# Kernel tuning notes

Measured on AMD Instinct MI355X. Metric: run time of the kernel, lower is better.

## Reference

```python
import jax, jax.numpy as jnp
import numpy as np

B, S, T, D = 16, 512, 16, 128
LN_EPS = 1e-5


def setup_inputs() -> dict:
    key = jax.random.key(0)
    k_x, k_h, k_w = jax.random.split(key, 3)
    x = jax.random.normal(k_x, (B, S, T, D), dtype=jnp.float32)
    # prev_hidden must be strictly positive (code takes its log)
    prev_hidden = jax.random.uniform(k_h, (B, 1, T, D), dtype=jnp.float32) * 0.9 + 0.05
    ln_gamma = jnp.ones((D,), jnp.float32)
    ln_beta = jnp.zeros((D,), jnp.float32)
    # torch Linear(dim, 2*dim): store as (D, 2D) for x @ W
    W = jax.random.normal(k_w, (D, 2 * D), dtype=jnp.float32) * (1.0 / np.sqrt(D))
    b = jnp.zeros((2 * D,), jnp.float32)
    return {"x": x, "prev_hidden": prev_hidden, "ln_gamma": ln_gamma,
            "ln_beta": ln_beta, "W": W, "b": b}


def _g_act_log(h):
    # log of G activation: x>=0 -> log(relu(x)+0.5); x<0 -> -softplus(-x)
    return jnp.where(h >= 0, jnp.log(jax.nn.relu(h) + 0.5), -jax.nn.softplus(-h))


def reference(x, prev_hidden, ln_gamma, ln_beta, W, b):
    seq_len = x.shape[1]
    # LayerNorm over last dim
    mu = jnp.mean(x, axis=-1, keepdims=True)
    var = jnp.var(x, axis=-1, keepdims=True)
    xn = (x - mu) * jax.lax.rsqrt(var + LN_EPS) * ln_gamma + ln_beta
    gh = jnp.einsum('bstd,de->bste', xn, W) + b  # (B,S,T,2D)
    gate, hidden = jnp.split(gh, 2, axis=-1)
    # parallel (seq_len > 1) log-space path
    log_coeffs = -jax.nn.softplus(gate)          # log(1 - z)
    log_z = -jax.nn.softplus(-gate)              # log z
    log_values = log_z + _g_act_log(hidden)      # (B,S,T,D)
    # prepend prev_hidden: values get log(h0), coeffs get zero pad
    log_values = jnp.concatenate([jnp.log(prev_hidden), log_values], axis=1)
    zero_pad = jnp.zeros_like(log_coeffs[:, :1])
    log_coeffs = jnp.concatenate([zero_pad, log_coeffs], axis=1)
    # Heinsen associative scan in log space
    a_star = jnp.cumsum(log_coeffs, axis=1)
    log_h0_plus_b_star = jax.lax.cumlogsumexp(log_values - a_star, axis=1)
    out = jnp.exp(a_star + log_h0_plus_b_star)
    out = out[:, -seq_len:]
    next_prev_hidden = out[:, -1:]
    return out, next_prev_hidden
```

## Files before the change

kernel.cpp:

```cpp
#include <hip/hip_runtime.h>
#include <hip/hip_bf16.h>
#include <stdint.h>

#define BB 16
#define SS 512
#define TT 16
#define DD 128
#define CH 64
#define NCH (SS/CH)
#define LN_EPS 1e-5f

typedef __attribute__((ext_vector_type(8))) short short8;
typedef __attribute__((ext_vector_type(4))) float f32x4;

static __device__ __forceinline__ uint32_t cvt_pk_bf16(float lo, float hi) {
    uint32_t r;
    asm("v_cvt_pk_bf16_f32 %0, %1, %2" : "=v"(r) : "v"(lo), "v"(hi));
    return r;
}

#define BAR() do {                                            \
    asm volatile("s_waitcnt lgkmcnt(0)" ::: "memory");        \
    __builtin_amdgcn_s_barrier();                             \
    asm volatile("" ::: "memory");                            \
} while (0)

__global__ __launch_bounds__(512, 2) void fused_mingru(
    const float* __restrict__ x, const float* __restrict__ prevh,
    const float* __restrict__ gamma, const float* __restrict__ beta,
    const float* __restrict__ W, const float* __restrict__ bias,
    float* __restrict__ out, float* __restrict__ nexth)
{
    __shared__ __align__(16) unsigned char xnb[2][CH*256];

    const int tid  = threadIdx.x;
    const int w    = tid >> 6;
    const int lane = tid & 63;
    const int l15  = lane & 15;
    const int lhi  = lane >> 4;

    const int bt = blockIdx.x;
    const size_t rowstride = (size_t)TT * DD;
    const size_t base_bt   = ((size_t)(bt >> 4) * SS * TT + (bt & 15)) * DD;

    const int r_ln = tid >> 3;
    const int c8   = tid & 7;
    const int slot_p = ((r_ln >> 2) & 3)*16 + (r_ln >> 4)*4 + (r_ln & 3);
    const int keyx   = slot_p & 7;
    const float* xp0 = x + base_bt + (size_t)r_ln * rowstride + c8*16;

    f32x4 px0, px1, px2, px3;
    auto issuePx = [&](int st) {
        const float* xp = xp0 + (size_t)st * CH * rowstride;
        px0 = *(const f32x4*)(xp + 0);
        px1 = *(const f32x4*)(xp + 4);
        px2 = *(const f32x4*)(xp + 8);
        px3 = *(const f32x4*)(xp + 12);
    };
    issuePx(0);

    short8 wfr[2][4];
    float  bs2[2];
    #pragma unroll
    for (int ni = 0; ni < 2; ++ni) {
        const int col = (ni ? 128 : 0) + w*16 + l15;
        float acc = 0.0f;
        #pragma unroll
        for (int kt = 0; kt < 4; ++kt) {
            union { short8 s8; uint32_t u[4]; } fr;
            #pragma unroll
            for (int p = 0; p < 4; ++p) {
                const int k0 = kt*32 + lhi*8 + 2*p;
                const float w0 = W[(size_t)k0*256 + col];
                const float w1 = W[(size_t)(k0+1)*256 + col];
                acc = fmaf(beta[k0],   w0, acc);
                acc = fmaf(beta[k0+1], w1, acc);
                fr.u[p] = cvt_pk_bf16(gamma[k0]*w0, gamma[k0+1]*w1);
            }
            wfr[ni][kt] = fr.s8;
        }
        acc += __shfl_xor(acc, 16);
        acc += __shfl_xor(acc, 32);
        bs2[ni] = bias[col] + acc;
    }

    float hM = prevh[(size_t)bt*128 + w*16 + l15];

    auto phaseLN = [&](int st) {
        float s1 = px0.x+px0.y+px0.z+px0.w + px1.x+px1.y+px1.z+px1.w
                 + px2.x+px2.y+px2.z+px2.w + px3.x+px3.y+px3.z+px3.w;
        float s2 = px0.x*px0.x+px0.y*px0.y+px0.z*px0.z+px0.w*px0.w
                 + px1.x*px1.x+px1.y*px1.y+px1.z*px1.z+px1.w*px1.w
                 + px2.x*px2.x+px2.y*px2.y+px2.z*px2.z+px2.w*px2.w
                 + px3.x*px3.x+px3.y*px3.y+px3.z*px3.z+px3.w*px3.w;
        s1 += __shfl_xor(s1, 1); s2 += __shfl_xor(s2, 1);
        s1 += __shfl_xor(s1, 2); s2 += __shfl_xor(s2, 2);
        s1 += __shfl_xor(s1, 4); s2 += __shfl_xor(s2, 4);
        const float mu = s1 * (1.0f/128.0f);
        const float rs = rsqrtf(s2 * (1.0f/128.0f) - mu*mu + LN_EPS);
        unsigned char* row = xnb[st & 1] + slot_p*256;
        union { short8 s8; uint32_t u[4]; } a, b2;
        a.u[0]  = cvt_pk_bf16((px0.x-mu)*rs, (px0.y-mu)*rs);
        a.u[1]  = cvt_pk_bf16((px0.z-mu)*rs, (px0.w-mu)*rs);
        a.u[2]  = cvt_pk_bf16((px1.x-mu)*rs, (px1.y-mu)*rs);
        a.u[3]  = cvt_pk_bf16((px1.z-mu)*rs, (px1.w-mu)*rs);
        b2.u[0] = cvt_pk_bf16((px2.x-mu)*rs, (px2.y-mu)*rs);
        b2.u[1] = cvt_pk_bf16((px2.z-mu)*rs, (px2.w-mu)*rs);
        b2.u[2] = cvt_pk_bf16((px3.x-mu)*rs, (px3.y-mu)*rs);
        b2.u[3] = cvt_pk_bf16((px3.z-mu)*rs, (px3.w-mu)*rs);
        *(short8*)(row + (((2*c8)     ^ keyx) << 4)) = a.s8;
        *(short8*)(row + (((2*c8 + 1) ^ keyx) << 4)) = b2.s8;
    };

    auto phaseG = [&](int st) {
        const unsigned char* xb = xnb[st & 1];
        float Cc[16], Cv[16];
        #pragma unroll
        for (int mt = 0; mt < 4; ++mt) {
            const unsigned char* rowp = xb + (mt*16 + l15)*256;
            short8 af[4];
            #pragma unroll
            for (int kt = 0; kt < 4; ++kt) {
                const int c = (kt << 2) | lhi;
                af[kt] = *(const short8*)(rowp + ((c ^ (l15 & 7)) << 4));
            }
            f32x4 ag = (f32x4)(0.f), ah = (f32x4)(0.f);
            #pragma unroll
            for (int kt = 0; kt < 4; ++kt) {
                ag = __builtin_amdgcn_mfma_f32_16x16x32_bf16(af[kt], wfr[0][kt], ag, 0, 0, 0);
                ah = __builtin_amdgcn_mfma_f32_16x16x32_bf16(af[kt], wfr[1][kt], ah, 0, 0, 0);
            }
            #pragma unroll
            for (int j = 0; j < 4; ++j) {
                const float g  = ag[j] + bs2[0];
                const float hh = ah[j] + bs2[1];
                const float cc = 1.0f / (1.0f + __expf(g));
                const float ga = (hh >= 0.0f) ? (hh + 0.5f)
                                              : (1.0f / (1.0f + __expf(-hh)));
                Cc[mt*4 + j] = cc;
                Cv[mt*4 + j] = (1.0f - cc) * ga;
            }
        }
        #pragma unroll
        for (int i = 1; i < 16; ++i) {
            Cv[i] = fmaf(Cc[i], Cv[i-1], Cv[i]);
            Cc[i] = Cc[i] * Cc[i-1];
        }
        float Ic = Cc[15], Iv = Cv[15];
        float pc = __shfl_up(Ic, 16), pv = __shfl_up(Iv, 16);
        if (lhi >= 1) { Iv = fmaf(Ic, pv, Iv); Ic *= pc; }
        pc = __shfl_up(Ic, 32); pv = __shfl_up(Iv, 32);
        if (lhi >= 2) { Iv = fmaf(Ic, pv, Iv); Ic *= pc; }
        float Ec = __shfl_up(Ic, 16), Ev = __shfl_up(Iv, 16);
        if (lhi == 0) { Ec = 1.0f; Ev = 0.0f; }
        const float Mc = __shfl(Ic, 48 + l15);
        const float Mv = __shfl(Iv, 48 + l15);
        const float hE = fmaf(Ec, hM, Ev);
        float* op = out + base_bt + (size_t)(st*CH + lhi*16) * rowstride + w*16 + l15;
        #pragma unroll
        for (int i = 0; i < 16; ++i)
            op[(size_t)i * rowstride] = fmaf(Cc[i], hE, Cv[i]);
        hM = fmaf(Mc, hM, Mv);
    };

    phaseLN(0);
    issuePx(1);
    BAR();

    for (int st = 0; st < NCH; ++st) {
        phaseG(st);
        if (st + 1 < NCH) {
            phaseLN(st + 1);
            if (st + 2 < NCH) issuePx(st + 2);
        }
        BAR();
    }

    if (lane < 16)
        nexth[(size_t)bt*128 + w*16 + lane] = hM;
}

extern "C" void kernel_launch(void* const* d_in, const int* in_sizes, int n_in,
                              void* d_out, int out_size, void* d_ws, size_t ws_size,
                              hipStream_t stream) {
    const float* x     = (const float*)d_in[0];
    const float* prevh = (const float*)d_in[1];
    const float* gamma = (const float*)d_in[2];
    const float* beta  = (const float*)d_in[3];
    const float* W     = (const float*)d_in[4];
    const float* bias  = (const float*)d_in[5];

    float* out   = (float*)d_out;
    float* nexth = out + (size_t)BB*SS*TT*DD;

    fused_mingru<<<BB*TT, 512, 0, stream>>>(x, prevh, gamma, beta, W, bias,
                                            out, nexth);
}
```

Before: 41.93 us.

## Software-pipeline chunk scan compute ahead of output tail with double-buffered packages

Splits the per-chunk work into a compute stage (MFMA, activations, intra-chunk scan) and a tail stage (apply carried hidden state and store outputs). Chunk s+1 is now computed before chunk s's tail runs, with results held in two alternating register packages. This breaks the serial dependence on hM so the stores and the next chunk's MFMA work can overlap. The change also switches to an explicit waves_per_eu(2,2) attribute and adds a sched_barrier after the x loads. It roughly doubles the live register state, which risks spills or lower occupancy.

```diff
diff --git a/kernel.cpp b/kernel.cpp
--- a/kernel.cpp
+++ b/kernel.cpp
@@ -25,7 +25,9 @@
     asm volatile("" ::: "memory");                            \
 } while (0)
 
-__global__ __launch_bounds__(512, 2) void fused_mingru(
+__global__ __launch_bounds__(512)
+__attribute__((amdgpu_waves_per_eu(2, 2)))
+void fused_mingru(
     const float* __restrict__ x, const float* __restrict__ prevh,
     const float* __restrict__ gamma, const float* __restrict__ beta,
     const float* __restrict__ W, const float* __restrict__ bias,
@@ -56,6 +58,7 @@
         px1 = *(const f32x4*)(xp + 4);
         px2 = *(const f32x4*)(xp + 8);
         px3 = *(const f32x4*)(xp + 12);
+        __builtin_amdgcn_sched_barrier(0);
     };
     issuePx(0);
 
@@ -112,9 +115,11 @@
         *(short8*)(row + (((2*c8 + 1) ^ keyx) << 4)) = b2.s8;
     };
 
-    auto phaseG = [&](int st) {
+    struct Pkg { float Cc[16], Cv[16], Ec, Ev, Mc, Mv; };
+    Pkg pkA, pkB;
+
+    auto computePkg = [&](int st, Pkg& P) {
         const unsigned char* xb = xnb[st & 1];
-        float Cc[16], Cv[16];
         #pragma unroll
         for (int mt = 0; mt < 4; ++mt) {
             const unsigned char* rowp = xb + (mt*16 + l15)*256;
@@ -137,42 +142,55 @@
                 const float cc = 1.0f / (1.0f + __expf(g));
                 const float ga = (hh >= 0.0f) ? (hh + 0.5f)
                                               : (1.0f / (1.0f + __expf(-hh)));
-                Cc[mt*4 + j] = cc;
-                Cv[mt*4 + j] = (1.0f - cc) * ga;
+                P.Cc[mt*4 + j] = cc;
+                P.Cv[mt*4 + j] = (1.0f - cc) * ga;
             }
         }
         #pragma unroll
         for (int i = 1; i < 16; ++i) {
-            Cv[i] = fmaf(Cc[i], Cv[i-1], Cv[i]);
-            Cc[i] = Cc[i] * Cc[i-1];
+            P.Cv[i] = fmaf(P.Cc[i], P.Cv[i-1], P.Cv[i]);
+            P.Cc[i] = P.Cc[i] * P.Cc[i-1];
         }
-        float Ic = Cc[15], Iv = Cv[15];
+        float Ic = P.Cc[15], Iv = P.Cv[15];
         float pc = __shfl_up(Ic, 16), pv = __shfl_up(Iv, 16);
         if (lhi >= 1) { Iv = fmaf(Ic, pv, Iv); Ic *= pc; }
         pc = __shfl_up(Ic, 32); pv = __shfl_up(Iv, 32);
         if (lhi >= 2) { Iv = fmaf(Ic, pv, Iv); Ic *= pc; }
         float Ec = __shfl_up(Ic, 16), Ev = __shfl_up(Iv, 16);
         if (lhi == 0) { Ec = 1.0f; Ev = 0.0f; }
-        const float Mc = __shfl(Ic, 48 + l15);
-        const float Mv = __shfl(Iv, 48 + l15);
-        const float hE = fmaf(Ec, hM, Ev);
+        P.Ec = Ec; P.Ev = Ev;
+        P.Mc = __shfl(Ic, 48 + l15);
+        P.Mv = __shfl(Iv, 48 + l15);
+    };
+
+    auto tail = [&](int st, Pkg& P) {
+        const float hE = fmaf(P.Ec, hM, P.Ev);
         float* op = out + base_bt + (size_t)(st*CH + lhi*16) * rowstride + w*16 + l15;
         #pragma unroll
         for (int i = 0; i < 16; ++i)
-            op[(size_t)i * rowstride] = fmaf(Cc[i], hE, Cv[i]);
-        hM = fmaf(Mc, hM, Mv);
+            op[(size_t)i * rowstride] = fmaf(P.Cc[i], hE, P.Cv[i]);
+        hM = fmaf(P.Mc, hM, P.Mv);
     };
 
     phaseLN(0);
     issuePx(1);
     BAR();
-
-    for (int st = 0; st < NCH; ++st) {
-        phaseG(st);
-        if (st + 1 < NCH) {
-            phaseLN(st + 1);
-            if (st + 2 < NCH) issuePx(st + 2);
-        }
+    computePkg(0, pkA);
+    phaseLN(1);
+    issuePx(2);
+    BAR();
+
+    #pragma unroll
+    for (int s2 = 0; s2 < NCH; s2 += 2) {
+        if (s2 + 1 < NCH) computePkg(s2 + 1, pkB);
+        tail(s2, pkA);
+        if (s2 + 2 < NCH) phaseLN(s2 + 2);
+        if (s2 + 3 < NCH) issuePx(s2 + 3);
+        BAR();
+        if (s2 + 2 < NCH) computePkg(s2 + 2, pkA);
+        tail(s2 + 1, pkB);
+        if (s2 + 3 < NCH) phaseLN(s2 + 3);
+        if (s2 + 4 < NCH) issuePx(s2 + 4);
         BAR();
     }
 
```

Measured after the change: 42.46 us. About the same (+1.3%).

## Split each (b,t) sequence across two 256-thread blocks by output-column half

Applied to the files above, without the earlier changes.

Each (b,t) scan is now handled by two blocks of 256 threads, each computing 64 of the 128 output channels, doubling the grid to 512 blocks. Every block still loads and LayerNorms the full 64-row x chunk, with 4 threads per row and 32 floats each, so x reads and LN work are duplicated. The aim is more blocks to fill the 256 CUs and less serial work per block, at the cost of twice the x traffic and more registers per thread for the larger LN load.

```diff
diff --git a/kernel.cpp b/kernel.cpp
--- a/kernel.cpp
+++ b/kernel.cpp
@@ -25,7 +25,7 @@
     asm volatile("" ::: "memory");                            \
 } while (0)
 
-__global__ __launch_bounds__(512, 2) void fused_mingru(
+__global__ __launch_bounds__(256, 2) void fused_mingru(
     const float* __restrict__ x, const float* __restrict__ prevh,
     const float* __restrict__ gamma, const float* __restrict__ beta,
     const float* __restrict__ W, const float* __restrict__ bias,
@@ -39,23 +39,23 @@
     const int l15  = lane & 15;
     const int lhi  = lane >> 4;
 
-    const int bt = blockIdx.x;
+    const int bt   = blockIdx.x >> 1;
+    const int half = blockIdx.x & 1;
     const size_t rowstride = (size_t)TT * DD;
     const size_t base_bt   = ((size_t)(bt >> 4) * SS * TT + (bt & 15)) * DD;
 
-    const int r_ln = tid >> 3;
-    const int c8   = tid & 7;
+    const int r_ln = tid >> 2;
+    const int c4   = tid & 3;
     const int slot_p = ((r_ln >> 2) & 3)*16 + (r_ln >> 4)*4 + (r_ln & 3);
     const int keyx   = slot_p & 7;
-    const float* xp0 = x + base_bt + (size_t)r_ln * rowstride + c8*16;
+    const float* xp0 = x + base_bt + (size_t)r_ln * rowstride + c4*32;
 
-    f32x4 px0, px1, px2, px3;
+    f32x4 px[8];
     auto issuePx = [&](int st) {
         const float* xp = xp0 + (size_t)st * CH * rowstride;
-        px0 = *(const f32x4*)(xp + 0);
-        px1 = *(const f32x4*)(xp + 4);
-        px2 = *(const f32x4*)(xp + 8);
-        px3 = *(const f32x4*)(xp + 12);
+        #pragma unroll
+        for (int q = 0; q < 8; ++q)
+            px[q] = *(const f32x4*)(xp + q*4);
     };
     issuePx(0);
 
@@ -63,7 +63,7 @@
     float  bs2[2];
     #pragma unroll
     for (int ni = 0; ni < 2; ++ni) {
-        const int col = (ni ? 128 : 0) + w*16 + l15;
+        const int col = (ni ? 128 : 0) + half*64 + w*16 + l15;
         float acc = 0.0f;
         #pragma unroll
         for (int kt = 0; kt < 4; ++kt) {
@@ -84,32 +84,31 @@
         bs2[ni] = bias[col] + acc;
     }
 
-    float hM = prevh[(size_t)bt*128 + w*16 + l15];
+    float hM = prevh[(size_t)bt*128 + half*64 + w*16 + l15];
 
     auto phaseLN = [&](int st) {
-        float s1 = px0.x+px0.y+px0.z+px0.w + px1.x+px1.y+px1.z+px1.w
-                 + px2.x+px2.y+px2.z+px2.w + px3.x+px3.y+px3.z+px3.w;
-        float s2 = px0.x*px0.x+px0.y*px0.y+px0.z*px0.z+px0.w*px0.w
-                 + px1.x*px1.x+px1.y*px1.y+px1.z*px1.z+px1.w*px1.w
-                 + px2.x*px2.x+px2.y*px2.y+px2.z*px2.z+px2.w*px2.w
-                 + px3.x*px3.x+px3.y*px3.y+px3.z*px3.z+px3.w*px3.w;
+        float s1 = 0.f, s2 = 0.f;
+        #pragma unroll
+        for (int q = 0; q < 8; ++q) {
+            s1 += px[q].x + px[q].y + px[q].z + px[q].w;
+            s2 += px[q].x*px[q].x + px[q].y*px[q].y
+                + px[q].z*px[q].z + px[q].w*px[q].w;
+        }
         s1 += __shfl_xor(s1, 1); s2 += __shfl_xor(s2, 1);
         s1 += __shfl_xor(s1, 2); s2 += __shfl_xor(s2, 2);
-        s1 += __shfl_xor(s1, 4); s2 += __shfl_xor(s2, 4);
         const float mu = s1 * (1.0f/128.0f);
         const float rs = rsqrtf(s2 * (1.0f/128.0f) - mu*mu + LN_EPS);
         unsigned char* row = xnb[st & 1] + slot_p*256;
-        union { short8 s8; uint32_t u[4]; } a, b2;
-        a.u[0]  = cvt_pk_bf16((px0.x-mu)*rs, (px0.y-mu)*rs);
-        a.u[1]  = cvt_pk_bf16((px0.z-mu)*rs, (px0.w-mu)*rs);
-        a.u[2]  = cvt_pk_bf16((px1.x-mu)*rs, (px1.y-mu)*rs);
-        a.u[3]  = cvt_pk_bf16((px1.z-mu)*rs, (px1.w-mu)*rs);
-        b2.u[0] = cvt_pk_bf16((px2.x-mu)*rs, (px2.y-mu)*rs);
-        b2.u[1] = cvt_pk_bf16((px2.z-mu)*rs, (px2.w-mu)*rs);
-        b2.u[2] = cvt_pk_bf16((px3.x-mu)*rs, (px3.y-mu)*rs);
-        b2.u[3] = cvt_pk_bf16((px3.z-mu)*rs, (px3.w-mu)*rs);
-        *(short8*)(row + (((2*c8)     ^ keyx) << 4)) = a.s8;
-        *(short8*)(row + (((2*c8 + 1) ^ keyx) << 4)) = b2.s8;
+        #pragma unroll
+        for (int m = 0; m < 4; ++m) {
+            union { short8 s8; uint32_t u[4]; } a;
+            a.u[0] = cvt_pk_bf16((px[2*m].x  -mu)*rs, (px[2*m].y  -mu)*rs);
+            a.u[1] = cvt_pk_bf16((px[2*m].z  -mu)*rs, (px[2*m].w  -mu)*rs);
+            a.u[2] = cvt_pk_bf16((px[2*m+1].x-mu)*rs, (px[2*m+1].y-mu)*rs);
+            a.u[3] = cvt_pk_bf16((px[2*m+1].z-mu)*rs, (px[2*m+1].w-mu)*rs);
+            const int ci = c4*4 + m;
+            *(short8*)(row + ((ci ^ keyx) << 4)) = a.s8;
+        }
     };
 
     auto phaseG = [&](int st) {
@@ -156,7 +155,8 @@
         const float Mc = __shfl(Ic, 48 + l15);
         const float Mv = __shfl(Iv, 48 + l15);
         const float hE = fmaf(Ec, hM, Ev);
-        float* op = out + base_bt + (size_t)(st*CH + lhi*16) * rowstride + w*16 + l15;
+        float* op = out + base_bt + (size_t)(st*CH + lhi*16) * rowstride
+                  + half*64 + w*16 + l15;
         #pragma unroll
         for (int i = 0; i < 16; ++i)
             op[(size_t)i * rowstride] = fmaf(Cc[i], hE, Cv[i]);
@@ -177,7 +177,7 @@
     }
 
     if (lane < 16)
-        nexth[(size_t)bt*128 + w*16 + lane] = hM;
+        nexth[(size_t)bt*128 + half*64 + w*16 + lane] = hM;
 }
 
 extern "C" void kernel_launch(void* const* d_in, const int* in_sizes, int n_in,
@@ -193,6 +193,6 @@
     float* out   = (float*)d_out;
     float* nexth = out + (size_t)BB*SS*TT*DD;
 
-    fused_mingru<<<BB*TT, 512, 0, stream>>>(x, prevh, gamma, beta, W, bias,
-                                            out, nexth);
+    fused_mingru<<<BB*TT*2, 256, 0, stream>>>(x, prevh, gamma, beta, W, bias,
+                                              out, nexth);
 }
```

New measurement: 51.54 us. +22.9%, slower.

## Split each chunk's scan across two wave groups with 1024-thread blocks

Applied to the files above, without the earlier changes.

Blocks grow from 512 to 1024 threads. The two groups of 8 waves each handle half of a 64-row chunk: 32 rows each, with 8 scan steps per lane instead of 16. The chunk carry is exchanged through a small shared buffer, and a second barrier per chunk resolves the cross-group prefix. This halves per-thread serial work and register pressure so more waves can hide latency with only 256 blocks in the grid, at the cost of an extra barrier per chunk and redundant W fragment loads per group.

```diff
diff --git a/kernel.cpp b/kernel.cpp
--- a/kernel.cpp
+++ b/kernel.cpp
@@ -25,16 +25,19 @@
     asm volatile("" ::: "memory");                            \
 } while (0)
 
-__global__ __launch_bounds__(512, 2) void fused_mingru(
+__global__ __launch_bounds__(1024, 4) void fused_mingru(
     const float* __restrict__ x, const float* __restrict__ prevh,
     const float* __restrict__ gamma, const float* __restrict__ beta,
     const float* __restrict__ W, const float* __restrict__ bias,
     float* __restrict__ out, float* __restrict__ nexth)
 {
     __shared__ __align__(16) unsigned char xnb[2][CH*256];
+    __shared__ float2 Mex[2][8][16];
 
     const int tid  = threadIdx.x;
-    const int w    = tid >> 6;
+    const int wave = tid >> 6;
+    const int q    = wave >> 3;
+    const int w    = wave & 7;
     const int lane = tid & 63;
     const int l15  = lane & 15;
     const int lhi  = lane >> 4;
@@ -43,19 +46,19 @@
     const size_t rowstride = (size_t)TT * DD;
     const size_t base_bt   = ((size_t)(bt >> 4) * SS * TT + (bt & 15)) * DD;
 
-    const int r_ln = tid >> 3;
-    const int c8   = tid & 7;
-    const int slot_p = ((r_ln >> 2) & 3)*16 + (r_ln >> 4)*4 + (r_ln & 3);
+    const int r_ln = tid >> 4;
+    const int c16  = tid & 15;
+    const int remq = r_ln & 31;
+    const int slot_p = ((r_ln >> 5)*2 + ((remq >> 2) & 1))*16
+                     + (remq >> 3)*4 + (remq & 3);
     const int keyx   = slot_p & 7;
-    const float* xp0 = x + base_bt + (size_t)r_ln * rowstride + c8*16;
-
-    f32x4 px0, px1, px2, px3;
+    const float* xp0 = x + base_bt + (size_t)r_ln * rowstride + c16*8;
+
+    f32x4 pxa, pxb;
     auto issuePx = [&](int st) {
         const float* xp = xp0 + (size_t)st * CH * rowstride;
-        px0 = *(const f32x4*)(xp + 0);
-        px1 = *(const f32x4*)(xp + 4);
-        px2 = *(const f32x4*)(xp + 8);
-        px3 = *(const f32x4*)(xp + 12);
+        pxa = *(const f32x4*)(xp + 0);
+        pxb = *(const f32x4*)(xp + 4);
     };
     issuePx(0);
 
@@ -87,37 +90,30 @@
     float hM = prevh[(size_t)bt*128 + w*16 + l15];
 
     auto phaseLN = [&](int st) {
-        float s1 = px0.x+px0.y+px0.z+px0.w + px1.x+px1.y+px1.z+px1.w
-                 + px2.x+px2.y+px2.z+px2.w + px3.x+px3.y+px3.z+px3.w;
-        float s2 = px0.x*px0.x+px0.y*px0.y+px0.z*px0.z+px0.w*px0.w
-                 + px1.x*px1.x+px1.y*px1.y+px1.z*px1.z+px1.w*px1.w
-                 + px2.x*px2.x+px2.y*px2.y+px2.z*px2.z+px2.w*px2.w
-                 + px3.x*px3.x+px3.y*px3.y+px3.z*px3.z+px3.w*px3.w;
+        float s1 = pxa.x+pxa.y+pxa.z+pxa.w + pxb.x+pxb.y+pxb.z+pxb.w;
+        float s2 = pxa.x*pxa.x+pxa.y*pxa.y+pxa.z*pxa.z+pxa.w*pxa.w
+                 + pxb.x*pxb.x+pxb.y*pxb.y+pxb.z*pxb.z+pxb.w*pxb.w;
         s1 += __shfl_xor(s1, 1); s2 += __shfl_xor(s2, 1);
         s1 += __shfl_xor(s1, 2); s2 += __shfl_xor(s2, 2);
         s1 += __shfl_xor(s1, 4); s2 += __shfl_xor(s2, 4);
+        s1 += __shfl_xor(s1, 8); s2 += __shfl_xor(s2, 8);
         const float mu = s1 * (1.0f/128.0f);
         const float rs = rsqrtf(s2 * (1.0f/128.0f) - mu*mu + LN_EPS);
-        unsigned char* row = xnb[st & 1] + slot_p*256;
-        union { short8 s8; uint32_t u[4]; } a, b2;
-        a.u[0]  = cvt_pk_bf16((px0.x-mu)*rs, (px0.y-mu)*rs);
-        a.u[1]  = cvt_pk_bf16((px0.z-mu)*rs, (px0.w-mu)*rs);
-        a.u[2]  = cvt_pk_bf16((px1.x-mu)*rs, (px1.y-mu)*rs);
-        a.u[3]  = cvt_pk_bf16((px1.z-mu)*rs, (px1.w-mu)*rs);
-        b2.u[0] = cvt_pk_bf16((px2.x-mu)*rs, (px2.y-mu)*rs);
-        b2.u[1] = cvt_pk_bf16((px2.z-mu)*rs, (px2.w-mu)*rs);
-        b2.u[2] = cvt_pk_bf16((px3.x-mu)*rs, (px3.y-mu)*rs);
-        b2.u[3] = cvt_pk_bf16((px3.z-mu)*rs, (px3.w-mu)*rs);
-        *(short8*)(row + (((2*c8)     ^ keyx) << 4)) = a.s8;
-        *(short8*)(row + (((2*c8 + 1) ^ keyx) << 4)) = b2.s8;
-    };
-
-    auto phaseG = [&](int st) {
+        union { short8 s8; uint32_t u[4]; } a;
+        a.u[0] = cvt_pk_bf16((pxa.x-mu)*rs, (pxa.y-mu)*rs);
+        a.u[1] = cvt_pk_bf16((pxa.z-mu)*rs, (pxa.w-mu)*rs);
+        a.u[2] = cvt_pk_bf16((pxb.x-mu)*rs, (pxb.y-mu)*rs);
+        a.u[3] = cvt_pk_bf16((pxb.z-mu)*rs, (pxb.w-mu)*rs);
+        *(short8*)(xnb[st & 1] + slot_p*256 + ((c16 ^ keyx) << 4)) = a.s8;
+    };
+
+    float Cc[8], Cv[8], Ec, Ev;
+
+    auto part1 = [&](int st) {
         const unsigned char* xb = xnb[st & 1];
-        float Cc[16], Cv[16];
-        #pragma unroll
-        for (int mt = 0; mt < 4; ++mt) {
-            const unsigned char* rowp = xb + (mt*16 + l15)*256;
+        #pragma unroll
+        for (int mt = 0; mt < 2; ++mt) {
+            const unsigned char* rowp = xb + (((2*q + mt)*16 + l15))*256;
             short8 af[4];
             #pragma unroll
             for (int kt = 0; kt < 4; ++kt) {
@@ -142,25 +138,34 @@
             }
         }
         #pragma unroll
-        for (int i = 1; i < 16; ++i) {
+        for (int i = 1; i < 8; ++i) {
             Cv[i] = fmaf(Cc[i], Cv[i-1], Cv[i]);
             Cc[i] = Cc[i] * Cc[i-1];
         }
-        float Ic = Cc[15], Iv = Cv[15];
+        float Ic = Cc[7], Iv = Cv[7];
         float pc = __shfl_up(Ic, 16), pv = __shfl_up(Iv, 16);
         if (lhi >= 1) { Iv = fmaf(Ic, pv, Iv); Ic *= pc; }
         pc = __shfl_up(Ic, 32); pv = __shfl_up(Iv, 32);
         if (lhi >= 2) { Iv = fmaf(Ic, pv, Iv); Ic *= pc; }
-        float Ec = __shfl_up(Ic, 16), Ev = __shfl_up(Iv, 16);
+        Ec = __shfl_up(Ic, 16); Ev = __shfl_up(Iv, 16);
         if (lhi == 0) { Ec = 1.0f; Ev = 0.0f; }
         const float Mc = __shfl(Ic, 48 + l15);
         const float Mv = __shfl(Iv, 48 + l15);
-        const float hE = fmaf(Ec, hM, Ev);
-        float* op = out + base_bt + (size_t)(st*CH + lhi*16) * rowstride + w*16 + l15;
-        #pragma unroll
-        for (int i = 0; i < 16; ++i)
+        if (lane < 16) Mex[q][w][lane] = make_float2(Mc, Mv);
+    };
+
+    auto part2 = [&](int st) {
+        const float2 m0 = Mex[0][w][l15];
+        const float2 m1 = Mex[1][w][l15];
+        const float h0 = fmaf(m0.x, hM, m0.y);
+        const float X  = q ? h0 : hM;
+        const float hE = fmaf(Ec, X, Ev);
+        float* op = out + base_bt
+                  + (size_t)(st*CH + q*32 + lhi*8) * rowstride + w*16 + l15;
+        #pragma unroll
+        for (int i = 0; i < 8; ++i)
             op[(size_t)i * rowstride] = fmaf(Cc[i], hE, Cv[i]);
-        hM = fmaf(Mc, hM, Mv);
+        hM = fmaf(m1.x, h0, m1.y);
     };
 
     phaseLN(0);
@@ -168,15 +173,15 @@
     BAR();
 
     for (int st = 0; st < NCH; ++st) {
-        phaseG(st);
-        if (st + 1 < NCH) {
-            phaseLN(st + 1);
-            if (st + 2 < NCH) issuePx(st + 2);
-        }
+        part1(st);
+        if (st + 1 < NCH) phaseLN(st + 1);
+        BAR();
+        part2(st);
+        if (st + 2 < NCH) issuePx(st + 2);
         BAR();
     }
 
-    if (lane < 16)
+    if (q == 0 && lane < 16)
         nexth[(size_t)bt*128 + w*16 + lane] = hM;
 }
 
@@ -193,6 +198,6 @@
     float* out   = (float*)d_out;
     float* nexth = out + (size_t)BB*SS*TT*DD;
 
-    fused_mingru<<<BB*TT, 512, 0, stream>>>(x, prevh, gamma, beta, W, bias,
-                                            out, nexth);
+    fused_mingru<<<BB*TT, 1024, 0, stream>>>(x, prevh, gamma, beta, W, bias,
+                                             out, nexth);
 }
```

Measured after the change: 47.46 us. 13.2% more time.
